# Kernel tuning notes

Hardware: AMD Instinct MI355X
Metric: run time of the kernel (lower is better)

The kernel has to match this reference:

```python
import jax, jax.numpy as jnp
import numpy as np

DIM = 768
N_HEADS = 12
HEAD_DIM = DIM // N_HEADS
MLP_DIM = 3072
DEPTH = 12
B, N = 16, 512


def setup_inputs() -> dict:
    key = jax.random.key(0)
    ks = jax.random.split(key, 12)
    s = 0.02
    return {
        "x": jax.random.normal(ks[0], (B, N, DIM), dtype=jnp.float32),
        "ln_w": jnp.ones((DIM,), jnp.float32),
        "ln_b": jnp.zeros((DIM,), jnp.float32),
        "wq": jax.random.normal(ks[1], (DIM, DIM), jnp.float32) * s,
        "bq": jnp.zeros((DIM,), jnp.float32),
        "wk": jax.random.normal(ks[2], (DIM, DIM), jnp.float32) * s,
        "bk": jnp.zeros((DIM,), jnp.float32),
        "wv": jax.random.normal(ks[3], (DIM, DIM), jnp.float32) * s,
        "bv": jnp.zeros((DIM,), jnp.float32),
        "w1": jax.random.normal(ks[4], (DIM, MLP_DIM), jnp.float32) * s,
        "b1": jnp.zeros((MLP_DIM,), jnp.float32),
        "w2": jax.random.normal(ks[5], (MLP_DIM, DIM), jnp.float32) * s,
        "b2": jnp.zeros((DIM,), jnp.float32),
    }


def _layernorm(x, w, b):
    mu = jnp.mean(x, axis=-1, keepdims=True)
    var = jnp.var(x, axis=-1, keepdims=True)
    return (x - mu) * jax.lax.rsqrt(var + 1e-5) * w + b


def _mha(x, wq, bq, wk, bk, wv, bv):
    # x: [b, n, dim]; weights stored as [in, out]
    def heads(t):
        return t.reshape(B, N, N_HEADS, HEAD_DIM).transpose(0, 2, 1, 3)  # b h n d
    q = heads(x @ wq + bq)
    k = heads(x @ wk + bk)
    v = heads(x @ wv + bv)
    scores = jnp.einsum('bhqd,bhkd->bhqk', q, k) / np.sqrt(HEAD_DIM).astype(np.float32)
    attn = jax.nn.softmax(scores, axis=-1)
    o = jnp.einsum('bhqk,bhkd->bhqd', attn, v)
    return o.transpose(0, 2, 1, 3).reshape(B, N, DIM)


def reference(x, ln_w, ln_b, wq, bq, wk, bk, wv, bv, w1, b1, w2, b2):
    # Dropout is identity in eval mode. Same weights reused each depth iteration.
    for _ in range(DEPTH):
        x = _mha(_layernorm(x, ln_w, ln_b), wq, bq, wk, bk, wv, bv) + x
        h = _layernorm(x, ln_w, ln_b)
        h = jax.nn.gelu(h @ w1 + b1, approximate=False) @ w2 + b2
        x = h + x
    return x
```

## Files before the change

kernel.cpp:

```cpp
#include <hip/hip_runtime.h>

typedef __bf16 bf16x8 __attribute__((ext_vector_type(8)));
typedef float f32x4 __attribute__((ext_vector_type(4)));
typedef unsigned short ushort8_t __attribute__((ext_vector_type(8)));
typedef unsigned short ushort4_t __attribute__((ext_vector_type(4)));

#define MFMA16(a, b, c) __builtin_amdgcn_mfma_f32_16x16x32_bf16((a), (b), (c), 0, 0, 0)

#define GLOAD16(gp, lp)                                                        \
  __builtin_amdgcn_global_load_lds(                                            \
      (__attribute__((address_space(1))) void*)(gp),                           \
      (__attribute__((address_space(3))) void*)(lp), 16, 0, 0)

#define WAITVM(N) asm volatile("s_waitcnt vmcnt(" #N ")" ::: "memory")
#define WAITLGKM0 asm volatile("s_waitcnt lgkmcnt(0)" ::: "memory")

__device__ __forceinline__ unsigned short f2bf(float f) {
  unsigned u = __builtin_bit_cast(unsigned, f);
  return (unsigned short)((u + 0x7FFFu + ((u >> 16) & 1u)) >> 16);
}

__global__ __launch_bounds__(256) void transpose_f2b(
    const float* __restrict__ src, unsigned short* __restrict__ dst,
    int Kdim, int Ndim) {
  long i = (long)blockIdx.x * 256 + threadIdx.x;
  if (i >= (long)Kdim * Ndim) return;
  int n = (int)(i / Kdim);
  int kk = (int)(i - (long)n * Kdim);
  dst[i] = f2bf(src[(long)kk * Ndim + n]);
}

__global__ __launch_bounds__(256) void ln_kernel(
    const float* __restrict__ x, const float* __restrict__ gw,
    const float* __restrict__ gb, unsigned short* __restrict__ h) {
  const int row = blockIdx.x * 4 + (threadIdx.x >> 6);
  const int l = threadIdx.x & 63;
  const float* xr = x + (long)row * 768;
  f32x4 va[3];
#pragma unroll
  for (int i = 0; i < 3; i++) va[i] = *(const f32x4*)(xr + i * 256 + l * 4);
  float s = 0.f, ss = 0.f;
#pragma unroll
  for (int i = 0; i < 3; i++)
#pragma unroll
    for (int j = 0; j < 4; j++) {
      float t = va[i][j];
      s += t;
      ss += t * t;
    }
#pragma unroll
  for (int off = 1; off < 64; off <<= 1) {
    s += __shfl_xor(s, off, 64);
    ss += __shfl_xor(ss, off, 64);
  }
  const float mu = s * (1.f / 768.f);
  const float var = ss * (1.f / 768.f) - mu * mu;
  const float inv = rsqrtf(var + 1e-5f);
  unsigned short* hp = h + (long)row * 768;
#pragma unroll
  for (int i = 0; i < 3; i++) {
    f32x4 wv = *(const f32x4*)(gw + i * 256 + l * 4);
    f32x4 bv = *(const f32x4*)(gb + i * 256 + l * 4);
    ushort4_t o;
#pragma unroll
    for (int j = 0; j < 4; j++) o[j] = f2bf((va[i][j] - mu) * inv * wv[j] + bv[j]);
    *(ushort4_t*)(hp + i * 256 + l * 4) = o;
  }
}

enum { EPI_QKV = 0, EPI_GELU = 1, EPI_RES = 2 };

template <int EPI>
__global__ __launch_bounds__(512) void gemm256(
    const unsigned short* __restrict__ A, const unsigned short* __restrict__ BT,
    int K, const float* __restrict__ bb0, const float* __restrict__ bb1,
    const float* __restrict__ bb2, unsigned short* __restrict__ o0,
    unsigned short* __restrict__ o1, unsigned short* __restrict__ o2) {
  __shared__ unsigned short As[2][2][8192];
  __shared__ unsigned short Bs[2][2][8192];
  const int tid = threadIdx.x;
  const int w = tid >> 6, l = tid & 63;
  const int lr = l & 15, lg = l >> 4;
  const int wr = w >> 2, wc = w & 3;
  const int sK = (lr >> 1) & 3;

  const int nx = gridDim.x;
  const int nwg = nx * gridDim.y;
  int wg = blockIdx.y * nx + blockIdx.x;
  {
    const int qq = nwg >> 3, rr = nwg & 7;
    const int xcd = wg & 7, idx = wg >> 3;
    wg = (xcd < rr ? xcd * (qq + 1) : rr * (qq + 1) + (xcd - rr) * qq) + idx;
  }
  const int bx = wg % nx, by = wg / nx;
  const int m0 = by * 256, n0 = bx * 256;

  const int srow = tid >> 2;
  const int schunk = tid & 3;
  const int spos = schunk ^ ((tid >> 3) & 3);

  ushort8_t rgA[2][2], rgB[2][2];

  auto ldA = [&](int kt, int kk, ushort8_t (&rg)[2]) {
#pragma unroll
    for (int r2 = 0; r2 < 2; r2++)
      rg[r2] = *(const ushort8_t*)(A + (long)(m0 + r2 * 128 + srow) * K +
                                   kt * 64 + kk * 32 + schunk * 8);
  };
  auto ldB = [&](int kt, int kk, ushort8_t (&rg)[2]) {
#pragma unroll
    for (int r2 = 0; r2 < 2; r2++)
      rg[r2] = *(const ushort8_t*)(BT + (long)(n0 + r2 * 128 + srow) * K +
                                   kt * 64 + kk * 32 + schunk * 8);
  };
  auto wrA = [&](int s, int kk, ushort8_t (&rg)[2]) {
#pragma unroll
    for (int r2 = 0; r2 < 2; r2++)
      *(ushort8_t*)&As[s][kk][(r2 * 128 + srow) * 32 + spos * 8] = rg[r2];
  };
  auto wrB = [&](int s, int kk, ushort8_t (&rg)[2]) {
#pragma unroll
    for (int r2 = 0; r2 < 2; r2++)
      *(ushort8_t*)&Bs[s][kk][(r2 * 128 + srow) * 32 + spos * 8] = rg[r2];
  };

  f32x4 acc[8][4] = {};
  const int NT = K >> 6;

  ldA(0, 0, rgA[0]); ldB(0, 0, rgB[0]);
  ldA(0, 1, rgA[1]); ldB(0, 1, rgB[1]);
  WAITVM(4);
  wrA(0, 0, rgA[0]); wrB(0, 0, rgB[0]);
  ldA(1, 0, rgA[0]); ldB(1, 0, rgB[0]);
  WAITVM(4);
  wrA(0, 1, rgA[1]); wrB(0, 1, rgB[1]);
  ldA(1, 1, rgA[1]); ldB(1, 1, rgB[1]);

  for (int kt = 0; kt < NT; ++kt) {
    const int s = kt & 1;
#pragma unroll
    for (int kk = 0; kk < 2; ++kk) {
      if (kt < NT - 2) {
        WAITVM(4);
      } else if (kt == NT - 2) {
        if (kk == 0) { WAITVM(4); } else { WAITVM(0); }
      }
      if (kt + 1 < NT) {
        wrA(s ^ 1, kk, rgA[kk]);
        wrB(s ^ 1, kk, rgB[kk]);
      }
      if (kt + 2 < NT) {
        ldA(kt + 2, kk, rgA[kk]);
        ldB(kt + 2, kk, rgB[kk]);
      }
      WAITLGKM0;
      __builtin_amdgcn_sched_barrier(0);
      __builtin_amdgcn_s_barrier();
      __builtin_amdgcn_sched_barrier(0);
      bf16x8 b[4];
#pragma unroll
      for (int j = 0; j < 4; j++)
        b[j] = *(const bf16x8*)&Bs[s][kk][(wc * 64 + j * 16 + lr) * 32 +
                                          ((lg ^ sK) * 8)];
#pragma unroll
      for (int H = 0; H < 2; H++) {
        bf16x8 a[4];
#pragma unroll
        for (int i = 0; i < 4; i++)
          a[i] = *(const bf16x8*)&As[s][kk][(wr * 128 + H * 64 + i * 16 + lr) * 32 +
                                            ((lg ^ sK) * 8)];
        __builtin_amdgcn_s_setprio(1);
#pragma unroll
        for (int i = 0; i < 4; i++)
#pragma unroll
          for (int j = 0; j < 4; j++)
            acc[H * 4 + i][j] = MFMA16(a[i], b[j], acc[H * 4 + i][j]);
        __builtin_amdgcn_s_setprio(0);
      }
    }
  }

  if (EPI == EPI_QKV) {
    const int whichq = n0 / 768;
    const int cc0 = n0 - whichq * 768 + wc * 64;
    const float* bias = whichq == 0 ? bb0 : whichq == 1 ? bb1 : bb2;
    if (whichq < 2) {
      unsigned short* dst = whichq == 0 ? o0 : o1;
#pragma unroll
      for (int fm = 0; fm < 8; fm++) {
        const int r = m0 + wr * 128 + fm * 16 + lg * 4;
        const int bidx = r >> 9, nb = r & 511;
#pragma unroll
        for (int fn = 0; fn < 4; fn++) {
          const int cc = cc0 + fn * 16 + lr;
          const int hd = cc >> 6, d = cc & 63;
          const float bv = bias[cc];
          unsigned short* pp = &dst[((long)(bidx * 12 + hd) * 512 + nb) * 64 + d];
#pragma unroll
          for (int q = 0; q < 4; q++) pp[q * 64] = f2bf(acc[fm][fn][q] + bv);
        }
      }
    } else {
#pragma unroll
      for (int fm = 0; fm < 8; fm++) {
        const int r = m0 + wr * 128 + fm * 16 + lg * 4;
        const int bidx = r >> 9, nb = r & 511;
#pragma unroll
        for (int fn = 0; fn < 4; fn++) {
          const int cc = cc0 + fn * 16 + lr;
          const int hd = cc >> 6, d = cc & 63;
          const float bv = bias[cc];
          ushort4_t pk;
#pragma unroll
          for (int q = 0; q < 4; q++) pk[q] = f2bf(acc[fm][fn][q] + bv);
          *(ushort4_t*)(&o2[((long)(bidx * 12 + hd) * 64 + d) * 512 + nb]) = pk;
        }
      }
    }
  } else {
#pragma unroll
    for (int fm = 0; fm < 8; fm++) {
      const int r = m0 + wr * 128 + fm * 16 + lg * 4;
#pragma unroll
      for (int fn = 0; fn < 4; fn++) {
        const int c = n0 + wc * 64 + fn * 16 + lr;
        const float bv = bb0[c];
#pragma unroll
        for (int q = 0; q < 4; q++) {
          float v = acc[fm][fn][q] + bv;
          const float u = v * (0.7978845608f + 0.0356774081f * v * v);
          const float g = v / (1.0f + __expf(-2.0f * u));
          o0[(long)(r + q) * 3072 + c] = f2bf(g);
        }
      }
    }
  }
}

__global__ __launch_bounds__(256) void gemm_res(
    const unsigned short* __restrict__ A, const unsigned short* __restrict__ BT,
    int K, const float* __restrict__ bb0, const float* __restrict__ oFin,
    float* __restrict__ oFout) {
  constexpr int BM = 64;
  constexpr int ABUF = BM * 32;
  __shared__ unsigned short As[2][ABUF];
  __shared__ unsigned short Bs[2][128 * 32];
  const int tid = threadIdx.x;
  const int w = tid >> 6, l = tid & 63;
  const int lr = l & 15, lg = l >> 4;
  const int wr = w >> 1, wc = w & 1;

  const int nx = gridDim.x;
  const int nwg = nx * gridDim.y;
  int wg = blockIdx.y * nx + blockIdx.x;
  {
    const int qq = nwg >> 3, rr = nwg & 7;
    const int xcd = wg & 7, idx = wg >> 3;
    wg = (xcd < rr ? xcd * (qq + 1) : rr * (qq + 1) + (xcd - rr) * qq) + idx;
  }
  const int bx = wg % nx, by = wg / nx;
  const int m0 = by * BM, n0 = bx * 128;

  const unsigned short* Ag = A + (long)(m0 + w * 16 + (l >> 2)) * K + (l & 3) * 8;
  const unsigned short* Bg = BT + (long)(n0 + w * 32 + (l >> 2)) * K + (l & 3) * 8;
  unsigned short* AsW = &As[0][w * 16 * 32 + l * 8];
  unsigned short* BsW = &Bs[0][w * 1024 + l * 8];

  auto stage = [&](int buf, int kt) {
    const unsigned short* ag = Ag + kt * 32;
    const unsigned short* bg = Bg + kt * 32;
    GLOAD16(ag, AsW + buf * ABUF);
    GLOAD16(bg, BsW + buf * 4096);
    GLOAD16(bg + 16 * K, BsW + buf * 4096 + 512);
  };

  f32x4 acc[2][4] = {};
  const int nk = K >> 5;
  stage(0, 0);
  __syncthreads();
  for (int kt = 0; kt < nk; ++kt) {
    const int cur = kt & 1;
    if (kt + 1 < nk) stage(cur ^ 1, kt + 1);
    bf16x8 a[2], b[4];
#pragma unroll
    for (int i = 0; i < 2; i++)
      a[i] = *(const bf16x8*)(&As[cur][(wr * 32 + i * 16 + lr) * 32 + lg * 8]);
#pragma unroll
    for (int j = 0; j < 4; j++)
      b[j] = *(const bf16x8*)(&Bs[cur][(wc * 64 + j * 16 + lr) * 32 + lg * 8]);
#pragma unroll
    for (int i = 0; i < 2; i++)
#pragma unroll
      for (int j = 0; j < 4; j++) acc[i][j] = MFMA16(a[i], b[j], acc[i][j]);
    __syncthreads();
  }

#pragma unroll
  for (int i = 0; i < 2; i++) {
    const int r = m0 + wr * 32 + i * 16 + lg * 4;
#pragma unroll
    for (int j = 0; j < 4; j++) {
      const int c = n0 + wc * 64 + j * 16 + lr;
      const float bv = bb0[c];
#pragma unroll
      for (int q = 0; q < 4; q++) {
        const long addr = (long)(r + q) * 768 + c;
        oFout[addr] = acc[i][j][q] + bv + oFin[addr];
      }
    }
  }
}

__global__ __launch_bounds__(256) void attn_kernel(
    const unsigned short* __restrict__ qg, const unsigned short* __restrict__ kg,
    const unsigned short* __restrict__ vtg, float* __restrict__ x) {
  __shared__ unsigned short Sh[128 * 64];
  __shared__ unsigned short Ks[2][64 * 64];
  __shared__ unsigned short Vt[2][64 * 64];
  const int qt = blockIdx.x, h = blockIdx.y, b = blockIdx.z;
  const int bh = b * 12 + h;
  const int tid = threadIdx.x, w = tid >> 6, l = tid & 63;
  const int lr = l & 15, lg = l >> 4;
  const int fchunk = ((l & 7) ^ ((l >> 3) & 7)) * 8;
  const int rk = lr & 7;

  const unsigned short* qbase =
      qg + ((long)bh * 512 + qt * 128 + w * 32 + (l >> 3)) * 64 + fchunk;
  unsigned short* shW = &Sh[w * 2048 + l * 8];
#pragma unroll
  for (int cc = 0; cc < 4; cc++) GLOAD16(qbase + cc * 8 * 64, shW + cc * 512);

  const unsigned short* kbase =
      kg + ((long)bh * 512 + w * 16 + (l >> 3)) * 64 + fchunk;
  const unsigned short* vbase =
      vtg + ((long)bh * 64 + w * 16 + (l >> 3)) * 512 + fchunk;
  unsigned short* KsW = &Ks[0][w * 1024 + l * 8];
  unsigned short* VtW = &Vt[0][w * 1024 + l * 8];

  auto stageKV = [&](int buf, int kt) {
#pragma unroll
    for (int cc = 0; cc < 2; cc++) {
      GLOAD16(kbase + (kt * 64 + cc * 8) * 64, KsW + buf * 4096 + cc * 512);
      GLOAD16(vbase + cc * 8 * 512 + kt * 64, VtW + buf * 4096 + cc * 512);
    }
  };
  stageKV(0, 0);
  __syncthreads();

  bf16x8 qa[2][2];
#pragma unroll
  for (int mi = 0; mi < 2; mi++)
#pragma unroll
    for (int ds = 0; ds < 2; ds++) {
      qa[mi][ds] = *(const bf16x8*)(&Sh[(w * 32 + mi * 16 + lr) * 64 +
                                        ((ds * 4 + lg) ^ rk) * 8]);
#pragma unroll
      for (int e = 0; e < 8; e++)
        qa[mi][ds][e] = (__bf16)(0.125f * (float)qa[mi][ds][e]);
    }

  unsigned short* Pw = &Sh[w * 2048];
  float lsum[8] = {};
  f32x4 o[2][4] = {};

  for (int kt = 0; kt < 8; ++kt) {
    const int cur = kt & 1;
    if (kt < 7) stageKV(cur ^ 1, kt + 1);

    f32x4 s[2][4] = {};
#pragma unroll
    for (int ds = 0; ds < 2; ++ds) {
      bf16x8 kb[4];
#pragma unroll
      for (int nj = 0; nj < 4; nj++)
        kb[nj] = *(const bf16x8*)(&Ks[cur][(nj * 16 + lr) * 64 +
                                           ((ds * 4 + lg) ^ rk) * 8]);
#pragma unroll
      for (int mi = 0; mi < 2; mi++)
#pragma unroll
        for (int nj = 0; nj < 4; nj++) s[mi][nj] = MFMA16(qa[mi][ds], kb[nj], s[mi][nj]);
    }

#pragma unroll
    for (int mi = 0; mi < 2; mi++)
#pragma unroll
      for (int nj = 0; nj < 4; nj++) {
        const int cL = nj * 2 + (lr >> 3);
#pragma unroll
        for (int q = 0; q < 4; q++) {
          const int row = mi * 16 + lg * 4 + q;
          const float p = __expf(s[mi][nj][q]);
          lsum[mi * 4 + q] += p;
          Pw[row * 64 + ((cL ^ (row & 7)) * 8) + (lr & 7)] = f2bf(p);
        }
      }

#pragma unroll
    for (int ks = 0; ks < 2; ++ks) {
      bf16x8 pa[2], vb[4];
#pragma unroll
      for (int mi = 0; mi < 2; mi++)
        pa[mi] = *(const bf16x8*)(&Pw[(mi * 16 + lr) * 64 +
                                      ((ks * 4 + lg) ^ rk) * 8]);
#pragma unroll
      for (int dj = 0; dj < 4; dj++)
        vb[dj] = *(const bf16x8*)(&Vt[cur][(dj * 16 + lr) * 64 +
                                           ((ks * 4 + lg) ^ rk) * 8]);
#pragma unroll
      for (int mi = 0; mi < 2; mi++)
#pragma unroll
        for (int dj = 0; dj < 4; dj++) o[mi][dj] = MFMA16(pa[mi], vb[dj], o[mi][dj]);
    }
    __syncthreads();
  }

#pragma unroll
  for (int i = 0; i < 8; i++) {
#pragma unroll
    for (int off = 1; off < 16; off <<= 1) lsum[i] += __shfl_xor(lsum[i], off, 64);
  }

#pragma unroll
  for (int mi = 0; mi < 2; mi++) {
#pragma unroll
    for (int q = 0; q < 4; q++) {
      const int n = qt * 128 + w * 32 + mi * 16 + lg * 4 + q;
      const float inv = 1.0f / lsum[mi * 4 + q];
      const long base = ((long)(b * 512 + n)) * 768 + h * 64;
#pragma unroll
      for (int dj = 0; dj < 4; dj++) {
        const long a = base + dj * 16 + lr;
        x[a] = x[a] + o[mi][dj][q] * inv;
      }
    }
  }
}

extern "C" void kernel_launch(void* const* d_in, const int* in_sizes, int n_in,
                              void* d_out, int out_size, void* d_ws,
                              size_t ws_size, hipStream_t stream) {
  const float* x_in = (const float*)d_in[0];
  const float* ln_w = (const float*)d_in[1];
  const float* ln_b = (const float*)d_in[2];
  const float* wq = (const float*)d_in[3];
  const float* bq = (const float*)d_in[4];
  const float* wk = (const float*)d_in[5];
  const float* bk = (const float*)d_in[6];
  const float* wv = (const float*)d_in[7];
  const float* bv = (const float*)d_in[8];
  const float* w1 = (const float*)d_in[9];
  const float* b1 = (const float*)d_in[10];
  const float* w2 = (const float*)d_in[11];
  const float* b2 = (const float*)d_in[12];

  char* p = (char*)d_ws;
  float* xw = (float*)p;            p += 8192L * 768 * 4;
  unsigned short* hbuf = (unsigned short*)p;  p += 8192L * 768 * 2;
  unsigned short* wqkvT = (unsigned short*)p; p += 2304L * 768 * 2;
  unsigned short* w1T = (unsigned short*)p;   p += 3072L * 768 * 2;
  unsigned short* w2T = (unsigned short*)p;   p += 768L * 3072 * 2;
  unsigned short* qb = (unsigned short*)p;
  unsigned short* kb = qb + 6291456L;
  unsigned short* vt = kb + 6291456L;
  unsigned short* gbuf = qb;

  hipMemcpyAsync(xw, x_in, 8192L * 768 * 4, hipMemcpyDeviceToDevice, stream);

  transpose_f2b<<<(768 * 768 + 255) / 256, 256, 0, stream>>>(wq, wqkvT, 768, 768);
  transpose_f2b<<<(768 * 768 + 255) / 256, 256, 0, stream>>>(wk, wqkvT + 589824L, 768, 768);
  transpose_f2b<<<(768 * 768 + 255) / 256, 256, 0, stream>>>(wv, wqkvT + 1179648L, 768, 768);
  transpose_f2b<<<(768 * 3072 + 255) / 256, 256, 0, stream>>>(w1, w1T, 768, 3072);
  transpose_f2b<<<(768 * 3072 + 255) / 256, 256, 0, stream>>>(w2, w2T, 3072, 768);

  for (int layer = 0; layer < 12; ++layer) {
    ln_kernel<<<2048, 256, 0, stream>>>(xw, ln_w, ln_b, hbuf);
    gemm256<EPI_QKV><<<dim3(9, 32), 512, 0, stream>>>(
        hbuf, wqkvT, 768, bq, bk, bv, qb, kb, vt);
    attn_kernel<<<dim3(4, 12, 16), 256, 0, stream>>>(qb, kb, vt, xw);
    ln_kernel<<<2048, 256, 0, stream>>>(xw, ln_w, ln_b, hbuf);
    gemm256<EPI_GELU><<<dim3(12, 32), 512, 0, stream>>>(
        hbuf, w1T, 768, b1, nullptr, nullptr, gbuf, nullptr, nullptr);
    gemm_res<<<dim3(6, 128), 256, 0, stream>>>(
        gbuf, w2T, 3072, b2, xw, layer == 11 ? (float*)d_out : xw);
  }
}
```

Before: 2.814 ms.

## Switch gemm256 to direct global-to-LDS loads and double K-step in gemm_res

The 256x256 GEMM now stages tiles with global_load_lds straight into shared memory, replacing the register-staged path with its manual vmcnt waits and XOR swizzle. The loop uses one __syncthreads per 64-wide K step. gemm_res now consumes 64 K per iteration over two 32-wide sub-buffers, which halves its barrier count, and it gains setprio around the MFMAs. The intent is to cut register pressure, VGPR round-trips and synchronisation. The cost is that LDS reads are no longer swizzled, so bank conflicts may appear, and the prefetch depth is reduced.

```diff
diff --git a/kernel.cpp b/kernel.cpp
--- a/kernel.cpp
+++ b/kernel.cpp
@@ -11,9 +11,6 @@
   __builtin_amdgcn_global_load_lds(                                            \
       (__attribute__((address_space(1))) void*)(gp),                           \
       (__attribute__((address_space(3))) void*)(lp), 16, 0, 0)
-
-#define WAITVM(N) asm volatile("s_waitcnt vmcnt(" #N ")" ::: "memory")
-#define WAITLGKM0 asm volatile("s_waitcnt lgkmcnt(0)" ::: "memory")
 
 __device__ __forceinline__ unsigned short f2bf(float f) {
   unsigned u = __builtin_bit_cast(unsigned, f);
@@ -82,7 +79,6 @@
   const int w = tid >> 6, l = tid & 63;
   const int lr = l & 15, lg = l >> 4;
   const int wr = w >> 2, wc = w & 3;
-  const int sK = (lr >> 1) & 3;
 
   const int nx = gridDim.x;
   const int nwg = nx * gridDim.y;
@@ -97,86 +93,45 @@
 
   const int srow = tid >> 2;
   const int schunk = tid & 3;
-  const int spos = schunk ^ ((tid >> 3) & 3);
-
-  ushort8_t rgA[2][2], rgB[2][2];
-
-  auto ldA = [&](int kt, int kk, ushort8_t (&rg)[2]) {
-#pragma unroll
-    for (int r2 = 0; r2 < 2; r2++)
-      rg[r2] = *(const ushort8_t*)(A + (long)(m0 + r2 * 128 + srow) * K +
-                                   kt * 64 + kk * 32 + schunk * 8);
+  const unsigned short* Ag = A + (long)(m0 + srow) * K + schunk * 8;
+  const unsigned short* Bg = BT + (long)(n0 + srow) * K + schunk * 8;
+
+  auto stage = [&](int buf, int kt) {
+    const long ko = (long)kt * 64;
+#pragma unroll
+    for (int kk = 0; kk < 2; kk++) {
+#pragma unroll
+      for (int h = 0; h < 2; h++) {
+        GLOAD16(Ag + (long)(h * 128) * K + ko + kk * 32,
+                &As[buf][kk][h * 4096 + tid * 8]);
+        GLOAD16(Bg + (long)(h * 128) * K + ko + kk * 32,
+                &Bs[buf][kk][h * 4096 + tid * 8]);
+      }
+    }
   };
-  auto ldB = [&](int kt, int kk, ushort8_t (&rg)[2]) {
-#pragma unroll
-    for (int r2 = 0; r2 < 2; r2++)
-      rg[r2] = *(const ushort8_t*)(BT + (long)(n0 + r2 * 128 + srow) * K +
-                                   kt * 64 + kk * 32 + schunk * 8);
-  };
-  auto wrA = [&](int s, int kk, ushort8_t (&rg)[2]) {
-#pragma unroll
-    for (int r2 = 0; r2 < 2; r2++)
-      *(ushort8_t*)&As[s][kk][(r2 * 128 + srow) * 32 + spos * 8] = rg[r2];
-  };
-  auto wrB = [&](int s, int kk, ushort8_t (&rg)[2]) {
-#pragma unroll
-    for (int r2 = 0; r2 < 2; r2++)
-      *(ushort8_t*)&Bs[s][kk][(r2 * 128 + srow) * 32 + spos * 8] = rg[r2];
-  };
 
   f32x4 acc[8][4] = {};
-  const int NT = K >> 6;
-
-  ldA(0, 0, rgA[0]); ldB(0, 0, rgB[0]);
-  ldA(0, 1, rgA[1]); ldB(0, 1, rgB[1]);
-  WAITVM(4);
-  wrA(0, 0, rgA[0]); wrB(0, 0, rgB[0]);
-  ldA(1, 0, rgA[0]); ldB(1, 0, rgB[0]);
-  WAITVM(4);
-  wrA(0, 1, rgA[1]); wrB(0, 1, rgB[1]);
-  ldA(1, 1, rgA[1]); ldB(1, 1, rgB[1]);
-
-  for (int kt = 0; kt < NT; ++kt) {
-    const int s = kt & 1;
-#pragma unroll
-    for (int kk = 0; kk < 2; ++kk) {
-      if (kt < NT - 2) {
-        WAITVM(4);
-      } else if (kt == NT - 2) {
-        if (kk == 0) { WAITVM(4); } else { WAITVM(0); }
-      }
-      if (kt + 1 < NT) {
-        wrA(s ^ 1, kk, rgA[kk]);
-        wrB(s ^ 1, kk, rgB[kk]);
-      }
-      if (kt + 2 < NT) {
-        ldA(kt + 2, kk, rgA[kk]);
-        ldB(kt + 2, kk, rgB[kk]);
-      }
-      WAITLGKM0;
-      __builtin_amdgcn_sched_barrier(0);
-      __builtin_amdgcn_s_barrier();
-      __builtin_amdgcn_sched_barrier(0);
-      bf16x8 b[4];
+  const int nk = K >> 6;
+  stage(0, 0);
+  for (int kt = 0; kt < nk; ++kt) {
+    const int cur = kt & 1;
+    __syncthreads();
+    if (kt + 1 < nk) stage(cur ^ 1, kt + 1);
+#pragma unroll
+    for (int kk = 0; kk < 2; kk++) {
+      bf16x8 a[8], b[4];
+#pragma unroll
+      for (int i = 0; i < 8; i++)
+        a[i] = *(const bf16x8*)(&As[cur][kk][(wr * 128 + i * 16 + lr) * 32 + lg * 8]);
 #pragma unroll
       for (int j = 0; j < 4; j++)
-        b[j] = *(const bf16x8*)&Bs[s][kk][(wc * 64 + j * 16 + lr) * 32 +
-                                          ((lg ^ sK) * 8)];
-#pragma unroll
-      for (int H = 0; H < 2; H++) {
-        bf16x8 a[4];
-#pragma unroll
-        for (int i = 0; i < 4; i++)
-          a[i] = *(const bf16x8*)&As[s][kk][(wr * 128 + H * 64 + i * 16 + lr) * 32 +
-                                            ((lg ^ sK) * 8)];
-        __builtin_amdgcn_s_setprio(1);
-#pragma unroll
-        for (int i = 0; i < 4; i++)
-#pragma unroll
-          for (int j = 0; j < 4; j++)
-            acc[H * 4 + i][j] = MFMA16(a[i], b[j], acc[H * 4 + i][j]);
-        __builtin_amdgcn_s_setprio(0);
-      }
+        b[j] = *(const bf16x8*)(&Bs[cur][kk][(wc * 64 + j * 16 + lr) * 32 + lg * 8]);
+      __builtin_amdgcn_s_setprio(1);
+#pragma unroll
+      for (int i = 0; i < 8; i++)
+#pragma unroll
+        for (int j = 0; j < 4; j++) acc[i][j] = MFMA16(a[i], b[j], acc[i][j]);
+      __builtin_amdgcn_s_setprio(0);
     }
   }
 
@@ -242,9 +197,8 @@
     int K, const float* __restrict__ bb0, const float* __restrict__ oFin,
     float* __restrict__ oFout) {
   constexpr int BM = 64;
-  constexpr int ABUF = BM * 32;
-  __shared__ unsigned short As[2][ABUF];
-  __shared__ unsigned short Bs[2][128 * 32];
+  __shared__ unsigned short As[2][2][BM * 32];
+  __shared__ unsigned short Bs[2][2][128 * 32];
   const int tid = threadIdx.x;
   const int w = tid >> 6, l = tid & 63;
   const int lr = l & 15, lg = l >> 4;
@@ -263,36 +217,42 @@
 
   const unsigned short* Ag = A + (long)(m0 + w * 16 + (l >> 2)) * K + (l & 3) * 8;
   const unsigned short* Bg = BT + (long)(n0 + w * 32 + (l >> 2)) * K + (l & 3) * 8;
-  unsigned short* AsW = &As[0][w * 16 * 32 + l * 8];
-  unsigned short* BsW = &Bs[0][w * 1024 + l * 8];
 
   auto stage = [&](int buf, int kt) {
-    const unsigned short* ag = Ag + kt * 32;
-    const unsigned short* bg = Bg + kt * 32;
-    GLOAD16(ag, AsW + buf * ABUF);
-    GLOAD16(bg, BsW + buf * 4096);
-    GLOAD16(bg + 16 * K, BsW + buf * 4096 + 512);
+    const long ko = (long)kt * 64;
+#pragma unroll
+    for (int kk = 0; kk < 2; kk++) {
+      GLOAD16(Ag + ko + kk * 32, &As[buf][kk][w * 16 * 32 + l * 8]);
+#pragma unroll
+      for (int h = 0; h < 2; h++)
+        GLOAD16(Bg + (long)(h * 16) * K + ko + kk * 32,
+                &Bs[buf][kk][(w * 32 + h * 16) * 32 + l * 8]);
+    }
   };
 
   f32x4 acc[2][4] = {};
-  const int nk = K >> 5;
+  const int nk = K >> 6;
   stage(0, 0);
-  __syncthreads();
   for (int kt = 0; kt < nk; ++kt) {
     const int cur = kt & 1;
+    __syncthreads();
     if (kt + 1 < nk) stage(cur ^ 1, kt + 1);
-    bf16x8 a[2], b[4];
-#pragma unroll
-    for (int i = 0; i < 2; i++)
-      a[i] = *(const bf16x8*)(&As[cur][(wr * 32 + i * 16 + lr) * 32 + lg * 8]);
-#pragma unroll
-    for (int j = 0; j < 4; j++)
-      b[j] = *(const bf16x8*)(&Bs[cur][(wc * 64 + j * 16 + lr) * 32 + lg * 8]);
-#pragma unroll
-    for (int i = 0; i < 2; i++)
-#pragma unroll
-      for (int j = 0; j < 4; j++) acc[i][j] = MFMA16(a[i], b[j], acc[i][j]);
-    __syncthreads();
+#pragma unroll
+    for (int kk = 0; kk < 2; kk++) {
+      bf16x8 a[2], b[4];
+#pragma unroll
+      for (int i = 0; i < 2; i++)
+        a[i] = *(const bf16x8*)(&As[cur][kk][(wr * 32 + i * 16 + lr) * 32 + lg * 8]);
+#pragma unroll
+      for (int j = 0; j < 4; j++)
+        b[j] = *(const bf16x8*)(&Bs[cur][kk][(wc * 64 + j * 16 + lr) * 32 + lg * 8]);
+      __builtin_amdgcn_s_setprio(1);
+#pragma unroll
+      for (int i = 0; i < 2; i++)
+#pragma unroll
+        for (int j = 0; j < 4; j++) acc[i][j] = MFMA16(a[i], b[j], acc[i][j]);
+      __builtin_amdgcn_s_setprio(0);
+    }
   }
 
 #pragma unroll
```

Result: slower. 2.978 ms (+5.8%).
